# Kernel tuning notes

Hardware: AMD Instinct MI355X
Metric: run time of the kernel (lower is better)

## Reference

```python
import jax, jax.numpy as jnp
import numpy as np

NUM_CLASSES = 81
THRESHOLD = 0.5
NEGPOS_RATIO = 3
VAR = (0.1, 0.2)


def setup_inputs() -> dict:
    key = jax.random.key(0)
    kl, kc, kp1, kp2, kt1, kt2, klab = jax.random.split(key, 7)
    B, P, T = 64, 8732, 16
    loc_data = jax.random.normal(kl, (B, P, 4), jnp.float32)
    conf_data = jax.random.normal(kc, (B, P, NUM_CLASSES), jnp.float32)
    # priors in center-form (cx, cy, w, h), w/h strictly positive
    cxcy = jax.random.uniform(kp1, (P, 2), jnp.float32)
    wh = 0.05 + 0.45 * jax.random.uniform(kp2, (P, 2), jnp.float32)
    priors = jnp.concatenate([cxcy, wh], axis=1)
    # ground-truth boxes in point-form (xmin, ymin, xmax, ymax), valid in [0,1]
    mins = 0.7 * jax.random.uniform(kt1, (B, T, 2), jnp.float32)
    sizes = 0.05 + 0.25 * jax.random.uniform(kt2, (B, T, 2), jnp.float32)
    truth_boxes = jnp.concatenate([mins, mins + sizes], axis=-1)
    labels = jax.random.randint(klab, (B, T), 0, NUM_CLASSES - 1, jnp.int32)
    return {"loc_data": loc_data, "conf_data": conf_data, "priors": priors,
            "truth_boxes": truth_boxes, "labels": labels}


def _point_form(pr):
    # center-form -> point-form
    return jnp.concatenate([pr[:, :2] - pr[:, 2:] / 2, pr[:, :2] + pr[:, 2:] / 2], axis=1)


def _intersect(box_a, box_b):
    # [T,4] x [P,4] -> [T,P] intersection areas (the repo uses raw intersection, not IoU)
    max_xy = jnp.minimum(box_a[:, None, 2:], box_b[None, :, 2:])
    min_xy = jnp.maximum(box_a[:, None, :2], box_b[None, :, :2])
    inter = jnp.clip(max_xy - min_xy, 0.0, None)
    return inter[..., 0] * inter[..., 1]


def _encode(matched, priors):
    g_cxcy = (matched[:, :2] + matched[:, 2:4]) / 2 - priors[:, :2]
    g_cxcy = g_cxcy / (VAR[0] * priors[:, 2:])
    g_wh = (matched[:, 2:4] - matched[:, :2]) / priors[:, 2:]
    g_wh = jnp.log(g_wh + 1e-10) / VAR[1]
    return jnp.concatenate([g_cxcy, g_wh], axis=1)


def _match(truths, labels, priors):
    # truths [T,4] point-form, labels [T], priors [P,4] center-form
    T = truths.shape[0]
    P = priors.shape[0]
    overlaps = _intersect(truths, _point_form(priors))          # [T,P]
    best_prior_idx = jnp.argmax(overlaps, axis=1)               # [T]
    best_truth_overlap = jnp.max(overlaps, axis=0)              # [P]
    best_truth_idx = jnp.argmax(overlaps, axis=0)               # [P]
    # ensure each gt's best prior is kept (overlap forced to 2)
    best_truth_overlap = best_truth_overlap.at[best_prior_idx].set(2.0)
    hit = best_prior_idx[:, None] == jnp.arange(P)[None, :]     # [T,P]
    last_j = jnp.max(jnp.where(hit, jnp.arange(T)[:, None], -1), axis=0)  # [P]
    best_truth_idx = jnp.where(last_j >= 0, last_j, best_truth_idx)
    matches = truths[best_truth_idx]                            # [P,4]
    conf = jnp.where(best_truth_overlap < THRESHOLD, 0,
                     labels[best_truth_idx] + 1).astype(jnp.int32)
    return _encode(matches, priors), conf


def _smooth_l1(d):
    ad = jnp.abs(d)
    return jnp.where(ad < 1.0, 0.5 * d * d, ad - 0.5)


def _forward(loc_data, conf_data, priors, truth_boxes, labels):
    B, P, C = conf_data.shape
    loc_t, conf_t = jax.vmap(_match, in_axes=(0, 0, None))(truth_boxes, labels, priors)
    pos = conf_t > 0                                            # [B,P]
    num_pos = pos.sum(axis=1, keepdims=True)                    # [B,1]
    # localization smooth-L1 over positives (sum reduction)
    loss_l = jnp.sum(jnp.where(pos[..., None], _smooth_l1(loc_data - loc_t), 0.0))
    # per-prior cross-entropy
    logp = jax.nn.log_softmax(conf_data, axis=-1)               # [B,P,C]
    ce = -jnp.take_along_axis(logp, conf_t[..., None], axis=-1)[..., 0]  # [B,P]
    # hard-negative mining via double argsort rank
    mined = jnp.where(pos, 0.0, ce)
    order = jnp.argsort(-mined, axis=1)
    rank = jnp.argsort(order, axis=1)
    num_neg = jnp.clip(NEGPOS_RATIO * num_pos, None, P - 1)     # [B,1]
    neg = rank < num_neg
    loss_c = jnp.sum(jnp.where(pos | neg, ce, 0.0))
    N = jnp.maximum(num_pos.sum(), 1).astype(loc_data.dtype)
    return loss_l / N, loss_c / N


def reference(loc_data, conf_data, priors, truth_boxes, labels):
    return _forward(loc_data, conf_data, priors, truth_boxes, labels)
```

## Files before the change

### kernel.cpp

```cpp
#include <hip/hip_runtime.h>
#include <float.h>
#include <math.h>

#define B_NUM 64
#define P_NUM 8732
#define T_NUM 16
#define C_NUM 81
#define TPB1  512
#define RPB_LSE 128
#define NBLK_LSE ((B_NUM * P_NUM) / RPB_LSE)
#define GRID1 (B_NUM + NBLK_LSE)

__device__ __forceinline__ float smooth_l1(float d) {
    float ad = fabsf(d);
    return (ad < 1.0f) ? 0.5f * d * d : ad - 0.5f;
}

struct MatchSh {
    float s_t[T_NUM][4];
    int   s_lab[T_NUM];
    float s_bto[P_NUM];
    short s_bti[P_NUM];
    float s_rv[8 * T_NUM];
    int   s_ri[8 * T_NUM];
    int   s_bp[T_NUM];
    float s_red[8];
    int   s_redi[8];
};
struct LseSh {
    float s_c[RPB_LSE * C_NUM];
};
union __align__(16) Sh1 { MatchSh m; LseSh l; };

__global__ __launch_bounds__(TPB1) void k_fused1(
    const float* __restrict__ loc, const float* __restrict__ conf,
    const float* __restrict__ priors, const float* __restrict__ truths,
    const int* __restrict__ labels,
    int* __restrict__ conf_t, int* __restrict__ num_pos,
    float* __restrict__ loss_l_b, float* __restrict__ lse,
    float* __restrict__ negce, int* __restrict__ sel_ctr)
{
    __shared__ Sh1 sh;
    const int tid = threadIdx.x;
    const int lane = tid & 63, wv = tid >> 6;

    if (blockIdx.x < B_NUM) {
        const int b = blockIdx.x;
        if (b == 0 && tid == 0) *sel_ctr = 0;

        if (tid < T_NUM * 4) ((float*)sh.m.s_t)[tid] = truths[b * T_NUM * 4 + tid];
        if (tid < T_NUM)     sh.m.s_lab[tid] = labels[b * T_NUM + tid];
        __syncthreads();

        float bpv[T_NUM]; int bpi[T_NUM];
#pragma unroll
        for (int t = 0; t < T_NUM; ++t) { bpv[t] = -1.0f; bpi[t] = 0; }

        const float4* pr4 = (const float4*)priors;
        for (int p = tid; p < P_NUM; p += TPB1) {
            float4 pr = pr4[p];
            float px0 = pr.x - 0.5f * pr.z, py0 = pr.y - 0.5f * pr.w;
            float px1 = pr.x + 0.5f * pr.z, py1 = pr.y + 0.5f * pr.w;
            float btv = -1.0f; int bti = 0;
#pragma unroll
            for (int t = 0; t < T_NUM; ++t) {
                float ix = fminf(sh.m.s_t[t][2], px1) - fmaxf(sh.m.s_t[t][0], px0);
                float iy = fminf(sh.m.s_t[t][3], py1) - fmaxf(sh.m.s_t[t][1], py0);
                ix = fmaxf(ix, 0.0f); iy = fmaxf(iy, 0.0f);
                float ov = ix * iy;
                if (ov > btv) { btv = ov; bti = t; }
                if (ov > bpv[t]) { bpv[t] = ov; bpi[t] = p; }
            }
            sh.m.s_bto[p] = btv;
            sh.m.s_bti[p] = (short)bti;
        }
        __syncthreads();

#pragma unroll
        for (int t = 0; t < T_NUM; ++t) {
            float v = bpv[t]; int i = bpi[t];
#pragma unroll
            for (int off = 32; off > 0; off >>= 1) {
                float ov = __shfl_down(v, off);
                int   oi = __shfl_down(i, off);
                if (ov > v || (ov == v && oi < i)) { v = ov; i = oi; }
            }
            if (lane == 0) { sh.m.s_rv[wv * T_NUM + t] = v; sh.m.s_ri[wv * T_NUM + t] = i; }
        }
        __syncthreads();
        if (tid < T_NUM) {
            float v = sh.m.s_rv[tid]; int i = sh.m.s_ri[tid];
            for (int w = 1; w < 8; ++w) {
                float ov = sh.m.s_rv[w * T_NUM + tid]; int oi = sh.m.s_ri[w * T_NUM + tid];
                if (ov > v || (ov == v && oi < i)) { v = ov; i = oi; }
            }
            sh.m.s_bp[tid] = i;
        }
        __syncthreads();
        if (tid == 0) {
            for (int t = 0; t < T_NUM; ++t) {
                int pb = sh.m.s_bp[t];
                sh.m.s_bto[pb] = 2.0f;
                sh.m.s_bti[pb] = (short)t;
            }
        }
        __syncthreads();

        int cnt = 0; float lsum = 0.0f;
        const float4* loc4 = (const float4*)loc;
        for (int p = tid; p < P_NUM; p += TPB1) {
            float ovl = sh.m.s_bto[p];
            int ti = (int)sh.m.s_bti[p];
            int c = (ovl < 0.5f) ? 0 : (sh.m.s_lab[ti] + 1);
            conf_t[b * P_NUM + p] = c;
            if (c > 0) {
                cnt++;
                float4 pr = pr4[p];
                float mx0 = sh.m.s_t[ti][0], my0 = sh.m.s_t[ti][1];
                float mx1 = sh.m.s_t[ti][2], my1 = sh.m.s_t[ti][3];
                float gx = ((mx0 + mx1) * 0.5f - pr.x) / (0.1f * pr.z);
                float gy = ((my0 + my1) * 0.5f - pr.y) / (0.1f * pr.w);
                float gw = __logf((mx1 - mx0) / pr.z + 1e-10f) / 0.2f;
                float gh = __logf((my1 - my0) / pr.w + 1e-10f) / 0.2f;
                float4 l = loc4[b * P_NUM + p];
                lsum += smooth_l1(l.x - gx) + smooth_l1(l.y - gy)
                      + smooth_l1(l.z - gw) + smooth_l1(l.w - gh);
            }
        }
#pragma unroll
        for (int off = 32; off > 0; off >>= 1) {
            lsum += __shfl_down(lsum, off);
            cnt  += __shfl_down(cnt, off);
        }
        if (lane == 0) { sh.m.s_red[wv] = lsum; sh.m.s_redi[wv] = cnt; }
        __syncthreads();
        if (tid == 0) {
            float L = 0.0f; int C2 = 0;
            for (int w = 0; w < 8; ++w) { L += sh.m.s_red[w]; C2 += sh.m.s_redi[w]; }
            num_pos[b] = C2;
            loss_l_b[b] = L;
        }
    } else {
        const int blk = blockIdx.x - B_NUM;
        const int r0 = blk * RPB_LSE;

        const float4* src = (const float4*)(conf + (size_t)r0 * C_NUM);
        float4* dst = (float4*)sh.l.s_c;
#pragma unroll 2
        for (int i = tid; i < (RPB_LSE * C_NUM) / 4; i += TPB1) dst[i] = src[i];
        __syncthreads();

        const int row = tid >> 2, sub = tid & 3;
        const int st = sub * 21, en = (sub == 3) ? C_NUM : (st + 21);
        const float* rp = sh.l.s_c + row * C_NUM;

        float m = -FLT_MAX;
        for (int j = st; j < en; ++j) m = fmaxf(m, rp[j]);
        m = fmaxf(m, __shfl_xor(m, 1));
        m = fmaxf(m, __shfl_xor(m, 2));

        float s = 0.0f;
        for (int j = st; j < en; ++j) s += __expf(rp[j] - m);
        s += __shfl_xor(s, 1);
        s += __shfl_xor(s, 2);

        if (sub == 0) {
            int r = r0 + row;
            float l = m + __logf(s);
            lse[r] = l;
            negce[r] = l - rp[0];
        }
    }
}

#define ELEMS 9

__global__ __launch_bounds__(1024) void k_select(
    const float* __restrict__ negce, const float* __restrict__ lse,
    const float* __restrict__ conf, const int* __restrict__ conf_t,
    const int* __restrict__ num_pos, float* __restrict__ loss_l_b,
    float* __restrict__ negsum_b, float* __restrict__ pce_b,
    int* __restrict__ sel_ctr, float* __restrict__ out)
{
    __shared__ int   s_wh[16][256];
    __shared__ int   s_hist[256];
    __shared__ int   s_sel, s_rem;
    __shared__ float s_sv[16];
    __shared__ int   s_sc[16];
    __shared__ float s_pv[16];
    __shared__ int   s_last;

    const int b = blockIdx.x, tid = threadIdx.x;
    const int lane = tid & 63, wv = tid >> 6;

    unsigned int val[ELEMS];
    float pce = 0.0f;
#pragma unroll
    for (int i = 0; i < ELEMS; ++i) {
        int p = tid + i * 1024;
        unsigned int v = 0u;
        if (p < P_NUM) {
            size_t idx = (size_t)b * P_NUM + p;
            int c = conf_t[idx];
            if (c == 0) {
                v = __float_as_uint(negce[idx]);
            } else {
                pce += lse[idx] - conf[idx * C_NUM + c];
            }
        }
        val[i] = v;
    }

    int np = num_pos[b];
    int nn = 3 * np; if (nn > P_NUM - 1) nn = P_NUM - 1;

    if (nn > 0) {
        unsigned int prefix = 0;
        int k = nn;
#pragma unroll
        for (int shift = 24; shift >= 0; shift -= 8) {
            for (int i = tid; i < 16 * 256; i += 1024) ((int*)s_wh)[i] = 0;
            __syncthreads();
            const unsigned int pmask = (shift == 24) ? 0u : (0xFFFFFFFFu << (shift + 8));
#pragma unroll
            for (int i = 0; i < ELEMS; ++i) {
                unsigned int v = val[i];
                if ((v & pmask) == prefix)
                    atomicAdd(&s_wh[wv][(v >> shift) & 0xFF], 1);
            }
            __syncthreads();
            if (tid < 256) {
                int s = 0;
#pragma unroll
                for (int w = 0; w < 16; ++w) s += s_wh[w][tid];
                s_hist[tid] = s;
            }
            __syncthreads();
            if (wv == 0) {
                int c0 = s_hist[4 * lane + 0], c1 = s_hist[4 * lane + 1];
                int c2 = s_hist[4 * lane + 2], c3 = s_hist[4 * lane + 3];
                int t3 = c3, t2 = c2 + t3, t1 = c1 + t2, t0 = c0 + t1;
                int g = t0, G = g;
#pragma unroll
                for (int off = 1; off < 64; off <<= 1) {
                    int o = __shfl_down(G, off);
                    if (lane + off < 64) G += o;
                }
                int above = G - g;
                int suf0 = t0 + above, suf1 = t1 + above;
                int suf2 = t2 + above, suf3 = t3 + above, suf4 = above;
                if (suf0 >= k && suf1 < k) { s_sel = 4 * lane + 0; s_rem = k - suf1; }
                if (suf1 >= k && suf2 < k) { s_sel = 4 * lane + 1; s_rem = k - suf2; }
                if (suf2 >= k && suf3 < k) { s_sel = 4 * lane + 2; s_rem = k - suf3; }
                if (suf3 >= k && suf4 < k) { s_sel = 4 * lane + 3; s_rem = k - suf4; }
            }
            __syncthreads();
            prefix |= ((unsigned int)s_sel) << shift;
            k = s_rem;
        }

        float sgt = 0.0f; int cgt = 0;
#pragma unroll
        for (int i = 0; i < ELEMS; ++i) {
            unsigned int v = val[i];
            if (v > prefix) { sgt += __uint_as_float(v); cgt++; }
        }
#pragma unroll
        for (int off = 32; off > 0; off >>= 1) {
            sgt += __shfl_down(sgt, off);
            cgt += __shfl_down(cgt, off);
        }
        if (lane == 0) { s_sv[wv] = sgt; s_sc[wv] = cgt; }
        __syncthreads();
        if (tid == 0) {
            float S = 0.0f; int Ct = 0;
#pragma unroll
            for (int w = 0; w < 16; ++w) { S += s_sv[w]; Ct += s_sc[w]; }
            negsum_b[b] = S + (float)(nn - Ct) * __uint_as_float(prefix);
        }
    } else {
        if (tid == 0) negsum_b[b] = 0.0f;
    }

#pragma unroll
    for (int off = 32; off > 0; off >>= 1) pce += __shfl_down(pce, off);
    if (lane == 0) s_pv[wv] = pce;
    __syncthreads();
    if (tid == 0) {
        float PCE = 0.0f;
#pragma unroll
        for (int w = 0; w < 16; ++w) PCE += s_pv[w];
        pce_b[b] = PCE;
    }

    if (tid == 0) {
        __threadfence();
        int old = atomicAdd(sel_ctr, 1);
        s_last = (old == B_NUM - 1) ? 1 : 0;
    }
    __syncthreads();
    if (s_last) {
        __threadfence();
        float ll = 0.0f, ns = 0.0f, pc = 0.0f; int npos = 0;
        if (tid < B_NUM) {
            ll = loss_l_b[tid];
            ns = negsum_b[tid];
            pc = pce_b[tid];
            npos = num_pos[tid];
        }
#pragma unroll
        for (int off = 32; off > 0; off >>= 1) {
            ll += __shfl_down(ll, off);
            ns += __shfl_down(ns, off);
            pc += __shfl_down(pc, off);
            npos += __shfl_down(npos, off);
        }
        if (lane == 0) {
            ((float*)s_wh[0])[wv] = ll;
            ((float*)s_wh[1])[wv] = ns;
            ((float*)s_wh[2])[wv] = pc;
            s_wh[3][wv] = npos;
        }
        __syncthreads();
        if (tid == 0) {
            float LL = 0.0f, NS = 0.0f, PC = 0.0f; int NP = 0;
#pragma unroll
            for (int w = 0; w < 16; ++w) {
                LL += ((float*)s_wh[0])[w];
                NS += ((float*)s_wh[1])[w];
                PC += ((float*)s_wh[2])[w];
                NP += s_wh[3][w];
            }
            float N = (float)(NP > 1 ? NP : 1);
            out[0] = LL / N;
            out[1] = (PC + NS) / N;
        }
    }
}

extern "C" void kernel_launch(void* const* d_in, const int* in_sizes, int n_in,
                              void* d_out, int out_size, void* d_ws, size_t ws_size,
                              hipStream_t stream) {
    const float* loc    = (const float*)d_in[0];
    const float* conf   = (const float*)d_in[1];
    const float* priors = (const float*)d_in[2];
    const float* truths = (const float*)d_in[3];
    const int*   labels = (const int*)d_in[4];
    float* out = (float*)d_out;

    int*   ws_i = (int*)d_ws;
    float* ws_f = (float*)d_ws;
    int*   num_pos   = ws_i;
    float* loss_l_b  = ws_f + 64;
    float* negsum_b  = ws_f + 128;
    float* pce_b     = ws_f + 192;
    int*   sel_ctr   = ws_i + 256;
    int*   conf_t    = ws_i + 512;
    float* negce     = ws_f + 512 + B_NUM * P_NUM;
    float* lse       = ws_f + 512 + 2 * B_NUM * P_NUM;

    k_fused1<<<GRID1, TPB1, 0, stream>>>(loc, conf, priors, truths, labels,
                                         conf_t, num_pos, loss_l_b, lse, negce, sel_ctr);
    k_select<<<B_NUM, 1024, 0, stream>>>(negce, lse, conf, conf_t, num_pos,
                                         loss_l_b, negsum_b, pce_b, sel_ctr, out);
}
```

Before: 73.61 us.

## Load conf rows directly to registers and shrink match shared memory

The log-sum-exp blocks stop staging 128 rows of conf through shared memory and have each thread load its 20-element slice straight into registers with unaligned float4 loads. The match state per prior is packed into a single 16-bit word holding the positive flag and the truth index, replacing the separate float and short arrays. Together with a launch bound of four blocks per CU, this cuts shared memory use and should raise occupancy for the bandwidth-bound softmax pass. The risk is misaligned 16-byte global loads, since the row stride of 81 floats breaks float4 alignment.

```diff
diff --git a/kernel.cpp b/kernel.cpp
--- a/kernel.cpp
+++ b/kernel.cpp
@@ -6,8 +6,8 @@
 #define P_NUM 8732
 #define T_NUM 16
 #define C_NUM 81
-#define TPB1  512
-#define RPB_LSE 128
+#define TPB   512
+#define RPB_LSE (TPB / 4)
 #define NBLK_LSE ((B_NUM * P_NUM) / RPB_LSE)
 #define GRID1 (B_NUM + NBLK_LSE)
 
@@ -16,23 +16,22 @@
     return (ad < 1.0f) ? 0.5f * d * d : ad - 0.5f;
 }
 
+__device__ __forceinline__ float4 ldg4(const float* p) {
+    float4 v; __builtin_memcpy(&v, p, 16); return v;
+}
+
 struct MatchSh {
     float s_t[T_NUM][4];
     int   s_lab[T_NUM];
-    float s_bto[P_NUM];
-    short s_bti[P_NUM];
+    unsigned short s_m[P_NUM];
     float s_rv[8 * T_NUM];
     int   s_ri[8 * T_NUM];
     int   s_bp[T_NUM];
     float s_red[8];
     int   s_redi[8];
 };
-struct LseSh {
-    float s_c[RPB_LSE * C_NUM];
-};
-union __align__(16) Sh1 { MatchSh m; LseSh l; };
-
-__global__ __launch_bounds__(TPB1) void k_fused1(
+
+__global__ __launch_bounds__(TPB, 4) void k_fused1(
     const float* __restrict__ loc, const float* __restrict__ conf,
     const float* __restrict__ priors, const float* __restrict__ truths,
     const int* __restrict__ labels,
@@ -40,136 +39,139 @@
     float* __restrict__ loss_l_b, float* __restrict__ lse,
     float* __restrict__ negce, int* __restrict__ sel_ctr)
 {
-    __shared__ Sh1 sh;
+    __shared__ MatchSh shm;
     const int tid = threadIdx.x;
     const int lane = tid & 63, wv = tid >> 6;
 
-    if (blockIdx.x < B_NUM) {
-        const int b = blockIdx.x;
-        if (b == 0 && tid == 0) *sel_ctr = 0;
-
-        if (tid < T_NUM * 4) ((float*)sh.m.s_t)[tid] = truths[b * T_NUM * 4 + tid];
-        if (tid < T_NUM)     sh.m.s_lab[tid] = labels[b * T_NUM + tid];
-        __syncthreads();
-
-        float bpv[T_NUM]; int bpi[T_NUM];
-#pragma unroll
-        for (int t = 0; t < T_NUM; ++t) { bpv[t] = -1.0f; bpi[t] = 0; }
-
-        const float4* pr4 = (const float4*)priors;
-        for (int p = tid; p < P_NUM; p += TPB1) {
-            float4 pr = pr4[p];
-            float px0 = pr.x - 0.5f * pr.z, py0 = pr.y - 0.5f * pr.w;
-            float px1 = pr.x + 0.5f * pr.z, py1 = pr.y + 0.5f * pr.w;
-            float btv = -1.0f; int bti = 0;
-#pragma unroll
-            for (int t = 0; t < T_NUM; ++t) {
-                float ix = fminf(sh.m.s_t[t][2], px1) - fmaxf(sh.m.s_t[t][0], px0);
-                float iy = fminf(sh.m.s_t[t][3], py1) - fmaxf(sh.m.s_t[t][1], py0);
-                ix = fmaxf(ix, 0.0f); iy = fmaxf(iy, 0.0f);
-                float ov = ix * iy;
-                if (ov > btv) { btv = ov; bti = t; }
-                if (ov > bpv[t]) { bpv[t] = ov; bpi[t] = p; }
-            }
-            sh.m.s_bto[p] = btv;
-            sh.m.s_bti[p] = (short)bti;
-        }
-        __syncthreads();
-
-#pragma unroll
-        for (int t = 0; t < T_NUM; ++t) {
-            float v = bpv[t]; int i = bpi[t];
-#pragma unroll
-            for (int off = 32; off > 0; off >>= 1) {
-                float ov = __shfl_down(v, off);
-                int   oi = __shfl_down(i, off);
-                if (ov > v || (ov == v && oi < i)) { v = ov; i = oi; }
-            }
-            if (lane == 0) { sh.m.s_rv[wv * T_NUM + t] = v; sh.m.s_ri[wv * T_NUM + t] = i; }
-        }
-        __syncthreads();
-        if (tid < T_NUM) {
-            float v = sh.m.s_rv[tid]; int i = sh.m.s_ri[tid];
-            for (int w = 1; w < 8; ++w) {
-                float ov = sh.m.s_rv[w * T_NUM + tid]; int oi = sh.m.s_ri[w * T_NUM + tid];
-                if (ov > v || (ov == v && oi < i)) { v = ov; i = oi; }
-            }
-            sh.m.s_bp[tid] = i;
-        }
-        __syncthreads();
-        if (tid == 0) {
-            for (int t = 0; t < T_NUM; ++t) {
-                int pb = sh.m.s_bp[t];
-                sh.m.s_bto[pb] = 2.0f;
-                sh.m.s_bti[pb] = (short)t;
-            }
-        }
-        __syncthreads();
-
-        int cnt = 0; float lsum = 0.0f;
-        const float4* loc4 = (const float4*)loc;
-        for (int p = tid; p < P_NUM; p += TPB1) {
-            float ovl = sh.m.s_bto[p];
-            int ti = (int)sh.m.s_bti[p];
-            int c = (ovl < 0.5f) ? 0 : (sh.m.s_lab[ti] + 1);
-            conf_t[b * P_NUM + p] = c;
-            if (c > 0) {
-                cnt++;
-                float4 pr = pr4[p];
-                float mx0 = sh.m.s_t[ti][0], my0 = sh.m.s_t[ti][1];
-                float mx1 = sh.m.s_t[ti][2], my1 = sh.m.s_t[ti][3];
-                float gx = ((mx0 + mx1) * 0.5f - pr.x) / (0.1f * pr.z);
-                float gy = ((my0 + my1) * 0.5f - pr.y) / (0.1f * pr.w);
-                float gw = __logf((mx1 - mx0) / pr.z + 1e-10f) / 0.2f;
-                float gh = __logf((my1 - my0) / pr.w + 1e-10f) / 0.2f;
-                float4 l = loc4[b * P_NUM + p];
-                lsum += smooth_l1(l.x - gx) + smooth_l1(l.y - gy)
-                      + smooth_l1(l.z - gw) + smooth_l1(l.w - gh);
-            }
-        }
-#pragma unroll
-        for (int off = 32; off > 0; off >>= 1) {
-            lsum += __shfl_down(lsum, off);
-            cnt  += __shfl_down(cnt, off);
-        }
-        if (lane == 0) { sh.m.s_red[wv] = lsum; sh.m.s_redi[wv] = cnt; }
-        __syncthreads();
-        if (tid == 0) {
-            float L = 0.0f; int C2 = 0;
-            for (int w = 0; w < 8; ++w) { L += sh.m.s_red[w]; C2 += sh.m.s_redi[w]; }
-            num_pos[b] = C2;
-            loss_l_b[b] = L;
-        }
-    } else {
-        const int blk = blockIdx.x - B_NUM;
-        const int r0 = blk * RPB_LSE;
-
-        const float4* src = (const float4*)(conf + (size_t)r0 * C_NUM);
-        float4* dst = (float4*)sh.l.s_c;
-#pragma unroll 2
-        for (int i = tid; i < (RPB_LSE * C_NUM) / 4; i += TPB1) dst[i] = src[i];
-        __syncthreads();
-
-        const int row = tid >> 2, sub = tid & 3;
-        const int st = sub * 21, en = (sub == 3) ? C_NUM : (st + 21);
-        const float* rp = sh.l.s_c + row * C_NUM;
-
-        float m = -FLT_MAX;
-        for (int j = st; j < en; ++j) m = fmaxf(m, rp[j]);
+    if (blockIdx.x >= B_NUM) {
+        const int r = (blockIdx.x - B_NUM) * RPB_LSE + (tid >> 2);
+        const int sub = tid & 3;
+        const float* rp = conf + (size_t)r * C_NUM;
+        const float* q = rp + sub * 20;
+
+        float4 q0 = ldg4(q);
+        float4 q1 = ldg4(q + 4);
+        float4 q2 = ldg4(q + 8);
+        float4 q3 = ldg4(q + 12);
+        float4 q4 = ldg4(q + 16);
+        float e20 = (sub == 3) ? rp[80] : -FLT_MAX;
+
+        float m = fmaxf(fmaxf(fmaxf(q0.x, q0.y), fmaxf(q0.z, q0.w)),
+                        fmaxf(fmaxf(q1.x, q1.y), fmaxf(q1.z, q1.w)));
+        m = fmaxf(m, fmaxf(fmaxf(q2.x, q2.y), fmaxf(q2.z, q2.w)));
+        m = fmaxf(m, fmaxf(fmaxf(q3.x, q3.y), fmaxf(q3.z, q3.w)));
+        m = fmaxf(m, fmaxf(fmaxf(q4.x, q4.y), fmaxf(q4.z, q4.w)));
+        m = fmaxf(m, e20);
         m = fmaxf(m, __shfl_xor(m, 1));
         m = fmaxf(m, __shfl_xor(m, 2));
 
-        float s = 0.0f;
-        for (int j = st; j < en; ++j) s += __expf(rp[j] - m);
+        float s = __expf(q0.x - m) + __expf(q0.y - m) + __expf(q0.z - m) + __expf(q0.w - m)
+                + __expf(q1.x - m) + __expf(q1.y - m) + __expf(q1.z - m) + __expf(q1.w - m)
+                + __expf(q2.x - m) + __expf(q2.y - m) + __expf(q2.z - m) + __expf(q2.w - m)
+                + __expf(q3.x - m) + __expf(q3.y - m) + __expf(q3.z - m) + __expf(q3.w - m)
+                + __expf(q4.x - m) + __expf(q4.y - m) + __expf(q4.z - m) + __expf(q4.w - m);
+        if (sub == 3) s += __expf(e20 - m);
         s += __shfl_xor(s, 1);
         s += __shfl_xor(s, 2);
 
         if (sub == 0) {
-            int r = r0 + row;
             float l = m + __logf(s);
             lse[r] = l;
-            negce[r] = l - rp[0];
-        }
+            negce[r] = l - q0.x;
+        }
+        return;
+    }
+
+    const int b = blockIdx.x;
+    if (b == 0 && tid == 0) *sel_ctr = 0;
+
+    if (tid < T_NUM * 4) ((float*)shm.s_t)[tid] = truths[b * T_NUM * 4 + tid];
+    if (tid < T_NUM)     shm.s_lab[tid] = labels[b * T_NUM + tid];
+    __syncthreads();
+
+    float bpv[T_NUM]; int bpi[T_NUM];
+#pragma unroll
+    for (int t = 0; t < T_NUM; ++t) { bpv[t] = -1.0f; bpi[t] = 0; }
+
+    const float4* pr4 = (const float4*)priors;
+    for (int p = tid; p < P_NUM; p += TPB) {
+        float4 pr = pr4[p];
+        float px0 = pr.x - 0.5f * pr.z, py0 = pr.y - 0.5f * pr.w;
+        float px1 = pr.x + 0.5f * pr.z, py1 = pr.y + 0.5f * pr.w;
+        float btv = -1.0f; int bti = 0;
+#pragma unroll
+        for (int t = 0; t < T_NUM; ++t) {
+            float ix = fminf(shm.s_t[t][2], px1) - fmaxf(shm.s_t[t][0], px0);
+            float iy = fminf(shm.s_t[t][3], py1) - fmaxf(shm.s_t[t][1], py0);
+            ix = fmaxf(ix, 0.0f); iy = fmaxf(iy, 0.0f);
+            float ov = ix * iy;
+            if (ov > btv) { btv = ov; bti = t; }
+            if (ov > bpv[t]) { bpv[t] = ov; bpi[t] = p; }
+        }
+        shm.s_m[p] = (unsigned short)((btv >= 0.5f ? 0x8000 : 0) | bti);
+    }
+    __syncthreads();
+
+#pragma unroll
+    for (int t = 0; t < T_NUM; ++t) {
+        float v = bpv[t]; int i = bpi[t];
+#pragma unroll
+        for (int off = 32; off > 0; off >>= 1) {
+            float ov = __shfl_down(v, off);
+            int   oi = __shfl_down(i, off);
+            if (ov > v || (ov == v && oi < i)) { v = ov; i = oi; }
+        }
+        if (lane == 0) { shm.s_rv[wv * T_NUM + t] = v; shm.s_ri[wv * T_NUM + t] = i; }
+    }
+    __syncthreads();
+    if (tid < T_NUM) {
+        float v = shm.s_rv[tid]; int i = shm.s_ri[tid];
+        for (int w = 1; w < 8; ++w) {
+            float ov = shm.s_rv[w * T_NUM + tid]; int oi = shm.s_ri[w * T_NUM + tid];
+            if (ov > v || (ov == v && oi < i)) { v = ov; i = oi; }
+        }
+        shm.s_bp[tid] = i;
+    }
+    __syncthreads();
+    if (tid == 0) {
+        for (int t = 0; t < T_NUM; ++t)
+            shm.s_m[shm.s_bp[t]] = (unsigned short)(0x8000 | t);
+    }
+    __syncthreads();
+
+    int cnt = 0; float lsum = 0.0f;
+    const float4* loc4 = (const float4*)loc;
+    for (int p = tid; p < P_NUM; p += TPB) {
+        unsigned short mm = shm.s_m[p];
+        int ti = mm & 0x7FFF;
+        int c = (mm & 0x8000) ? (shm.s_lab[ti] + 1) : 0;
+        conf_t[(size_t)b * P_NUM + p] = c;
+        if (c > 0) {
+            cnt++;
+            float4 pr = pr4[p];
+            float mx0 = shm.s_t[ti][0], my0 = shm.s_t[ti][1];
+            float mx1 = shm.s_t[ti][2], my1 = shm.s_t[ti][3];
+            float gx = ((mx0 + mx1) * 0.5f - pr.x) / (0.1f * pr.z);
+            float gy = ((my0 + my1) * 0.5f - pr.y) / (0.1f * pr.w);
+            float gw = __logf((mx1 - mx0) / pr.z + 1e-10f) / 0.2f;
+            float gh = __logf((my1 - my0) / pr.w + 1e-10f) / 0.2f;
+            float4 l = loc4[(size_t)b * P_NUM + p];
+            lsum += smooth_l1(l.x - gx) + smooth_l1(l.y - gy)
+                  + smooth_l1(l.z - gw) + smooth_l1(l.w - gh);
+        }
+    }
+#pragma unroll
+    for (int off = 32; off > 0; off >>= 1) {
+        lsum += __shfl_down(lsum, off);
+        cnt  += __shfl_down(cnt, off);
+    }
+    if (lane == 0) { shm.s_red[wv] = lsum; shm.s_redi[wv] = cnt; }
+    __syncthreads();
+    if (tid == 0) {
+        float L = 0.0f; int C2 = 0;
+        for (int w = 0; w < 8; ++w) { L += shm.s_red[w]; C2 += shm.s_redi[w]; }
+        num_pos[b] = C2;
+        loss_l_b[b] = L;
     }
 }
 
@@ -359,8 +361,8 @@
     float* negce     = ws_f + 512 + B_NUM * P_NUM;
     float* lse       = ws_f + 512 + 2 * B_NUM * P_NUM;
 
-    k_fused1<<<GRID1, TPB1, 0, stream>>>(loc, conf, priors, truths, labels,
-                                         conf_t, num_pos, loss_l_b, lse, negce, sel_ctr);
+    k_fused1<<<GRID1, TPB, 0, stream>>>(loc, conf, priors, truths, labels,
+                                        conf_t, num_pos, loss_l_b, lse, negce, sel_ctr);
     k_select<<<B_NUM, 1024, 0, stream>>>(negce, lse, conf, conf_t, num_pos,
                                          loss_l_b, negsum_b, pce_b, sel_ctr, out);
 }
```

Result: faster. 65.09 us (-11.6%).
